# Optimization experiments

Measured on AMD Instinct MI355X. Metric: run time of the kernel, lower is better.

The kernel has to match this reference:

```python
import jax, jax.numpy as jnp
import numpy as np

M_COMP = 8      # number of output components m (n = m * tmax)
TMAX = 512
BS = 32
N = M_COMP * TMAX  # 4096


def setup_inputs() -> dict:
    key = jax.random.key(0)
    k1, k2, k3, k4 = jax.random.split(key, 4)
    # K must be symmetric positive definite for the Cholesky factorization.
    A = jax.random.normal(k1, (N, N), dtype=jnp.float32)
    K = A @ A.T / N + 1e-2 * jnp.eye(N, dtype=jnp.float32)
    # Sigma: diagonal measurement-noise covariance (positive diagonal).
    Sigma = jnp.diag(jax.random.uniform(k2, (N,), dtype=jnp.float32, minval=0.1, maxval=0.5))
    mu = jax.random.normal(k3, (N,), dtype=jnp.float32)
    Y = jax.random.normal(k4, (BS * N,), dtype=jnp.float32)
    return {"Y": Y, "mu": mu, "K": K, "Sigma": Sigma, "bs": BS, "tmax": TMAX}


def reference(Y, mu, K, Sigma, bs, tmax):
    n = mu.shape[0]  # m * tmax
    KS = K + Sigma
    # Chol_inv: inv = L^{-T} L^{-1} = (K + Sigma)^{-1}
    L = jnp.linalg.cholesky(KS)
    Linv = jnp.linalg.inv(L)
    inv = Linv.T @ Linv  # [n, n]
    # Block-diagonal quadratic form == sum of per-trajectory quadratic forms.
    diff = mu[None, :] - Y.reshape(bs, n)  # [bs, n]
    quad = jnp.einsum('bi,ij,bj->', diff, inv, diff)
    # log det(K + Sigma); slogdet is the stable equivalent (det > 0 for SPD).
    _, logdet = jnp.linalg.slogdet(KS)
    lml = (-quad / (2.0 * bs)
           - 0.5 * logdet
           - 0.5 * tmax * jnp.log(jnp.asarray(2.0 * np.pi, dtype=KS.dtype)))
    return -lml
```

## Files before the change

### kernel.cpp

```cpp
#include <hip/hip_runtime.h>
#include <math.h>

#define Nn 4096
#define BSc 32
#define NB 128
#define NBB 32
#define NBLK 33
#define NK 32
#define TILE_ELEMS (NB * NB)
#define NTILES 561

typedef float f32x4 __attribute__((ext_vector_type(4)));
typedef short bf16x8 __attribute__((ext_vector_type(8)));

__device__ __forceinline__ size_t tile_off(int i, int j) {
  return ((size_t)(j * NBLK - (j * (j - 1)) / 2 + (i - j))) * TILE_ELEMS;
}

__device__ __forceinline__ unsigned short f2bf(float f) {
  union { float f; unsigned int u; } v; v.f = f;
  unsigned int r = v.u + 0x7fffu + ((v.u >> 16) & 1u);
  return (unsigned short)(r >> 16);
}
__device__ __forceinline__ float bf2f(unsigned short b) {
  union { unsigned int u; float f; } v; v.u = ((unsigned int)b) << 16;
  return v.f;
}

__global__ __launch_bounds__(256) void prep(const float* __restrict__ Y,
                                            const float* __restrict__ mu,
                                            const float* __restrict__ Kp,
                                            const float* __restrict__ Sg,
                                            float* __restrict__ W) {
  int bid = blockIdx.x;
  int j = 0;
  while (j + 1 < NBLK) {
    int nxt = (j + 1) * NBLK - ((j + 1) * j) / 2;
    if (bid < nxt) break;
    ++j;
  }
  int start = j * NBLK - (j * (j - 1)) / 2;
  int i = j + (bid - start);
  float* T = W + tile_off(i, j);
  int tid = threadIdx.x;
  for (int idx = tid; idx < TILE_ELEMS; idx += 256) {
    int li = idx >> 7, lj = idx & 127;
    int gr = i * NB + li, gc = j * NB + lj;
    float v = 0.0f;
    if (gr < Nn) {
      v = Kp[(size_t)gr * Nn + gc];
      if (gr == gc) v += Sg[(size_t)gr * Nn + gr];
    } else {
      int b = gr - Nn;
      if (b < BSc && gc < Nn) v = mu[gc] - Y[(size_t)b * Nn + gc];
    }
    T[idx] = v;
  }
}

__global__ __launch_bounds__(256) void potf2(float* __restrict__ W, int k) {
  __shared__ float T[NB][NB + 1];
  __shared__ float dinv_sh[NBB];
  float* G = W + tile_off(k, k);
  int tid = threadIdx.x;
  for (int idx = tid; idx < TILE_ELEMS / 4; idx += 256) {
    float4 v = ((const float4*)G)[idx];
    int r = idx >> 5, c = (idx & 31) * 4;
    T[r][c] = v.x; T[r][c + 1] = v.y; T[r][c + 2] = v.z; T[r][c + 3] = v.w;
  }
  __syncthreads();
  int lane = tid & 63, wid = tid >> 6;
  for (int kb = 0; kb < 4; ++kb) {
    int o = kb * NBB;
    if (wid == 0) {
      int i = lane & 31;
      float cc[NBB];
#pragma unroll
      for (int p = 0; p < NBB; ++p) cc[p] = T[o + i][o + p];
#pragma unroll
      for (int j = 0; j < NBB; ++j) {
        float s = cc[j];
#pragma unroll
        for (int p = 0; p < NBB; ++p) {
          if (p < j) s -= cc[p] * __shfl(cc[p], j, 64);
        }
        float sj = __shfl(s, j, 64);
        float d = sqrtf(sj);
        if (i == j) cc[j] = d;
        else if (i > j) cc[j] = s / d;
      }
      if (lane < 32) {
#pragma unroll
        for (int p = 0; p < NBB; ++p) {
          if (p <= i) T[o + i][o + p] = cc[p];
        }
      }
    }
    __syncthreads();
    if (tid < NBB) dinv_sh[tid] = 1.0f / T[o + tid][o + tid];
    __syncthreads();
    int R = NB - o - NBB;
    if (R > 0) {
      if (tid < R) {
        int r = o + NBB + tid;
        float x[NBB];
#pragma unroll
        for (int p = 0; p < NBB; ++p) x[p] = T[r][o + p];
#pragma unroll
        for (int j = 0; j < NBB; ++j) {
          float s = x[j];
#pragma unroll
          for (int p = 0; p < NBB; ++p) {
            if (p < j) s -= x[p] * T[o + j][o + p];
          }
          x[j] = s * dinv_sh[j];
        }
#pragma unroll
        for (int p = 0; p < NBB; ++p) T[r][o + p] = x[p];
      }
      __syncthreads();
      int TL = R >> 2;
      int ntile = TL * (TL + 1) / 2;
      for (int t = tid; t < ntile; t += 256) {
        int ti = (int)((sqrtf(8.0f * t + 1.0f) - 1.0f) * 0.5f);
        while ((ti + 1) * (ti + 2) / 2 <= t) ++ti;
        while (ti * (ti + 1) / 2 > t) --ti;
        int tj = t - ti * (ti + 1) / 2;
        int tr = o + NBB + ti * 4, tc = o + NBB + tj * 4;
        float acc[4][4];
#pragma unroll
        for (int m = 0; m < 4; ++m)
#pragma unroll
          for (int n = 0; n < 4; ++n) acc[m][n] = 0.0f;
        for (int p = 0; p < NBB; ++p) {
          float a0 = T[tr][o + p], a1 = T[tr + 1][o + p],
                a2 = T[tr + 2][o + p], a3 = T[tr + 3][o + p];
          float b0 = T[tc][o + p], b1 = T[tc + 1][o + p],
                b2 = T[tc + 2][o + p], b3 = T[tc + 3][o + p];
          acc[0][0] += a0 * b0; acc[0][1] += a0 * b1; acc[0][2] += a0 * b2; acc[0][3] += a0 * b3;
          acc[1][0] += a1 * b0; acc[1][1] += a1 * b1; acc[1][2] += a1 * b2; acc[1][3] += a1 * b3;
          acc[2][0] += a2 * b0; acc[2][1] += a2 * b1; acc[2][2] += a2 * b2; acc[2][3] += a2 * b3;
          acc[3][0] += a3 * b0; acc[3][1] += a3 * b1; acc[3][2] += a3 * b2; acc[3][3] += a3 * b3;
        }
#pragma unroll
        for (int m = 0; m < 4; ++m)
#pragma unroll
          for (int n = 0; n < 4; ++n) T[tr + m][tc + n] -= acc[m][n];
      }
    }
    __syncthreads();
  }
  for (int idx = tid; idx < TILE_ELEMS; idx += 256) {
    int r = idx >> 7, c = idx & 127;
    if (c <= r) G[idx] = T[r][c];
  }
}

__global__ __launch_bounds__(256) void trsm(float* __restrict__ W,
                                            unsigned short* __restrict__ PH,
                                            unsigned short* __restrict__ PL,
                                            int k) {
  __shared__ float Td[NB][NB + 1];
  __shared__ float X[NB][NB + 1];
  __shared__ float dinv_sh[NB];
  int tid = threadIdx.x;
  int i = k + 1 + blockIdx.x;
  int rows = (i == NBLK - 1) ? BSc : NB;
  const float* Gd = W + tile_off(k, k);
  const float* Gx = W + tile_off(i, k);
  for (int idx = tid; idx < TILE_ELEMS / 4; idx += 256) {
    float4 v = ((const float4*)Gd)[idx];
    float4 u = ((const float4*)Gx)[idx];
    int r = idx >> 5, c = (idx & 31) * 4;
    Td[r][c] = v.x; Td[r][c + 1] = v.y; Td[r][c + 2] = v.z; Td[r][c + 3] = v.w;
    if (r < rows) { X[r][c] = u.x; X[r][c + 1] = u.y; X[r][c + 2] = u.z; X[r][c + 3] = u.w; }
    else          { X[r][c] = 0.0f; X[r][c + 1] = 0.0f; X[r][c + 2] = 0.0f; X[r][c + 3] = 0.0f; }
  }
  __syncthreads();
  if (tid < NB) dinv_sh[tid] = 1.0f / Td[tid][tid];
  __syncthreads();
  int rtile = (tid >> 3) * 4;
  int ctile = (tid & 7) * 4;
  for (int jb = 0; jb < 4; ++jb) {
    int o = jb * NBB;
    if (jb > 0) {
      float acc[4][4];
#pragma unroll
      for (int m = 0; m < 4; ++m)
#pragma unroll
        for (int n = 0; n < 4; ++n) acc[m][n] = 0.0f;
      for (int p = 0; p < o; ++p) {
        float a0 = X[rtile][p], a1 = X[rtile + 1][p],
              a2 = X[rtile + 2][p], a3 = X[rtile + 3][p];
        float b0 = Td[o + ctile][p], b1 = Td[o + ctile + 1][p],
              b2 = Td[o + ctile + 2][p], b3 = Td[o + ctile + 3][p];
        acc[0][0] += a0 * b0; acc[0][1] += a0 * b1; acc[0][2] += a0 * b2; acc[0][3] += a0 * b3;
        acc[1][0] += a1 * b0; acc[1][1] += a1 * b1; acc[1][2] += a1 * b2; acc[1][3] += a1 * b3;
        acc[2][0] += a2 * b0; acc[2][1] += a2 * b1; acc[2][2] += a2 * b2; acc[2][3] += a2 * b3;
        acc[3][0] += a3 * b0; acc[3][1] += a3 * b1; acc[3][2] += a3 * b2; acc[3][3] += a3 * b3;
      }
#pragma unroll
      for (int m = 0; m < 4; ++m)
#pragma unroll
        for (int n = 0; n < 4; ++n) X[rtile + m][o + ctile + n] -= acc[m][n];
      __syncthreads();
    }
    if (tid < NB) {
      int r = tid;
      float x[NBB];
#pragma unroll
      for (int p = 0; p < NBB; ++p) x[p] = X[r][o + p];
#pragma unroll
      for (int j = 0; j < NBB; ++j) {
        float s = x[j];
#pragma unroll
        for (int p = 0; p < NBB; ++p) {
          if (p < j) s -= x[p] * Td[o + j][o + p];
        }
        x[j] = s * dinv_sh[o + j];
      }
#pragma unroll
      for (int p = 0; p < NBB; ++p) X[r][o + p] = x[p];
    }
    __syncthreads();
  }
  int r = tid >> 1, hf = tid & 1;
  unsigned short* ph = PH + (size_t)i * TILE_ELEMS + (size_t)r * NB + hf * 64;
  unsigned short* pl = PL + (size_t)i * TILE_ELEMS + (size_t)r * NB + hf * 64;
#pragma unroll
  for (int ch = 0; ch < 8; ++ch) {
    unsigned short hb[8], lb[8];
#pragma unroll
    for (int e = 0; e < 8; ++e) {
      float v = X[r][hf * 64 + ch * 8 + e];
      unsigned short h = f2bf(v);
      hb[e] = h;
      lb[e] = f2bf(v - bf2f(h));
    }
    *reinterpret_cast<uint4*>(&ph[ch * 8]) = *reinterpret_cast<const uint4*>(hb);
    *reinterpret_cast<uint4*>(&pl[ch * 8]) = *reinterpret_cast<const uint4*>(lb);
  }
}

__global__ __launch_bounds__(256) void syrk(const unsigned short* __restrict__ PH,
                                            const unsigned short* __restrict__ PL,
                                            float* __restrict__ W, int k) {
  int i = k + 1 + blockIdx.x, j = k + 1 + blockIdx.y;
  if (i < j) return;
  const unsigned short* Ahg = PH + (size_t)i * TILE_ELEMS;
  const unsigned short* Alg = PL + (size_t)i * TILE_ELEMS;
  const unsigned short* Bhg = PH + (size_t)j * TILE_ELEMS;
  const unsigned short* Blg = PL + (size_t)j * TILE_ELEMS;
  float* C = W + tile_off(i, j);
  __shared__ unsigned short Ah[NB][40], Al[NB][40], Bh[NB][40], Bl[NB][40];
  int tid = threadIdx.x, lane = tid & 63, wid = tid >> 6;
  int wr = wid >> 1, wc = wid & 1, lm = lane & 15, lk = lane >> 4;
  f32x4 acc[4][4];
#pragma unroll
  for (int m = 0; m < 4; ++m)
#pragma unroll
    for (int n = 0; n < 4; ++n) acc[m][n] = (f32x4)0.0f;
  int r = tid >> 1, hf = tid & 1;
  for (int kb = 0; kb < 4; ++kb) {
    int kbase = kb * 32;
    if (kb) __syncthreads();
#pragma unroll
    for (int c = 0; c < 2; ++c) {
      int lc = (hf * 2 + c) * 8;
      int kc = kbase + lc;
      *reinterpret_cast<uint4*>(&Ah[r][lc]) = *reinterpret_cast<const uint4*>(&Ahg[(size_t)r * NB + kc]);
      *reinterpret_cast<uint4*>(&Al[r][lc]) = *reinterpret_cast<const uint4*>(&Alg[(size_t)r * NB + kc]);
      *reinterpret_cast<uint4*>(&Bh[r][lc]) = *reinterpret_cast<const uint4*>(&Bhg[(size_t)r * NB + kc]);
      *reinterpret_cast<uint4*>(&Bl[r][lc]) = *reinterpret_cast<const uint4*>(&Blg[(size_t)r * NB + kc]);
    }
    __syncthreads();
    bf16x8 ah[4], al[4], bh[4], bl[4];
#pragma unroll
    for (int mt = 0; mt < 4; ++mt) {
      int row = wr * 64 + mt * 16 + lm;
      ah[mt] = *reinterpret_cast<const bf16x8*>(&Ah[row][lk * 8]);
      al[mt] = *reinterpret_cast<const bf16x8*>(&Al[row][lk * 8]);
    }
#pragma unroll
    for (int nt = 0; nt < 4; ++nt) {
      int col = wc * 64 + nt * 16 + lm;
      bh[nt] = *reinterpret_cast<const bf16x8*>(&Bh[col][lk * 8]);
      bl[nt] = *reinterpret_cast<const bf16x8*>(&Bl[col][lk * 8]);
    }
#pragma unroll
    for (int mt = 0; mt < 4; ++mt)
#pragma unroll
      for (int nt = 0; nt < 4; ++nt) {
        acc[mt][nt] = __builtin_amdgcn_mfma_f32_16x16x32_bf16(ah[mt], bh[nt], acc[mt][nt], 0, 0, 0);
        acc[mt][nt] = __builtin_amdgcn_mfma_f32_16x16x32_bf16(al[mt], bh[nt], acc[mt][nt], 0, 0, 0);
        acc[mt][nt] = __builtin_amdgcn_mfma_f32_16x16x32_bf16(ah[mt], bl[nt], acc[mt][nt], 0, 0, 0);
      }
  }
#pragma unroll
  for (int mt = 0; mt < 4; ++mt)
#pragma unroll
    for (int nt = 0; nt < 4; ++nt) {
#pragma unroll
      for (int q = 0; q < 4; ++q) {
        int rr = wr * 64 + mt * 16 + lk * 4 + q;
        int cc = wc * 64 + nt * 16 + lm;
        C[rr * NB + cc] -= acc[mt][nt][q];
      }
    }
}

__global__ __launch_bounds__(256) void finalize(const float* __restrict__ W,
                                                const int* __restrict__ bsp,
                                                const int* __restrict__ tmaxp,
                                                float* __restrict__ out) {
  __shared__ float rl[4], rq[4];
  int tid = threadIdx.x;
  float lsum = 0.0f;
  for (int d = tid; d < Nn; d += 256) {
    int db = d >> 7, dl = d & 127;
    lsum += logf(W[tile_off(db, db) + (size_t)dl * NB + dl]);
  }
  float qsum = 0.0f;
  if (tid < BSc) qsum = W[tile_off(NBLK - 1, NBLK - 1) + (size_t)tid * NB + tid];
  for (int o = 32; o > 0; o >>= 1) {
    lsum += __shfl_down(lsum, o, 64);
    qsum += __shfl_down(qsum, o, 64);
  }
  int lane = tid & 63, wid = tid >> 6;
  if (lane == 0) { rl[wid] = lsum; rq[wid] = qsum; }
  __syncthreads();
  if (tid == 0) {
    float Lt = rl[0] + rl[1] + rl[2] + rl[3];
    float Qt = rq[0] + rq[1] + rq[2] + rq[3];
    float bsf = (float)bsp[0];
    float tmaxf = (float)tmaxp[0];
    out[0] = -Qt / (2.0f * bsf) + Lt + 0.5f * tmaxf * logf(6.283185307179586f);
  }
}

extern "C" void kernel_launch(void* const* d_in, const int* in_sizes, int n_in,
                              void* d_out, int out_size, void* d_ws, size_t ws_size,
                              hipStream_t stream) {
  const float* Y   = (const float*)d_in[0];
  const float* mu  = (const float*)d_in[1];
  const float* Kp  = (const float*)d_in[2];
  const float* Sg  = (const float*)d_in[3];
  const int*   bsp = (const int*)d_in[4];
  const int*   tmp_= (const int*)d_in[5];
  float* W = (float*)d_ws;
  unsigned short* PH = (unsigned short*)(W + (size_t)NTILES * TILE_ELEMS);
  unsigned short* PL = PH + (size_t)NBLK * TILE_ELEMS;
  float* out = (float*)d_out;

  prep<<<NTILES, 256, 0, stream>>>(Y, mu, Kp, Sg, W);

  for (int k = 0; k < NK; ++k) {
    potf2<<<1, 256, 0, stream>>>(W, k);
    int T = NBLK - (k + 1);
    trsm<<<T, 256, 0, stream>>>(W, PH, PL, k);
    dim3 g(T, T);
    syrk<<<g, 256, 0, stream>>>(PH, PL, W, k);
  }
  finalize<<<1, 256, 0, stream>>>(W, bsp, tmp_, out);
}
```

Baseline: 4.060 ms.

## Fuse diagonal-block Cholesky into TRSM panel kernel, recomputing per block

Removes the separate single-block potf2 launch. Each trsm block now redundantly factors the diagonal tile in shared memory before doing its triangular solve, and block 0 writes the diagonal into a side array Ld that finalize uses for the log-determinant. This cuts one serialized launch and one global round trip per step, in exchange for every block repeating the same factorization. Several loops also get unroll 1 pragmas, likely to limit register pressure in the larger fused kernel.

```diff
diff --git a/kernel.cpp b/kernel.cpp
--- a/kernel.cpp
+++ b/kernel.cpp
@@ -58,108 +58,11 @@
   }
 }
 
-__global__ __launch_bounds__(256) void potf2(float* __restrict__ W, int k) {
-  __shared__ float T[NB][NB + 1];
-  __shared__ float dinv_sh[NBB];
-  float* G = W + tile_off(k, k);
-  int tid = threadIdx.x;
-  for (int idx = tid; idx < TILE_ELEMS / 4; idx += 256) {
-    float4 v = ((const float4*)G)[idx];
-    int r = idx >> 5, c = (idx & 31) * 4;
-    T[r][c] = v.x; T[r][c + 1] = v.y; T[r][c + 2] = v.z; T[r][c + 3] = v.w;
-  }
-  __syncthreads();
-  int lane = tid & 63, wid = tid >> 6;
-  for (int kb = 0; kb < 4; ++kb) {
-    int o = kb * NBB;
-    if (wid == 0) {
-      int i = lane & 31;
-      float cc[NBB];
-#pragma unroll
-      for (int p = 0; p < NBB; ++p) cc[p] = T[o + i][o + p];
-#pragma unroll
-      for (int j = 0; j < NBB; ++j) {
-        float s = cc[j];
-#pragma unroll
-        for (int p = 0; p < NBB; ++p) {
-          if (p < j) s -= cc[p] * __shfl(cc[p], j, 64);
-        }
-        float sj = __shfl(s, j, 64);
-        float d = sqrtf(sj);
-        if (i == j) cc[j] = d;
-        else if (i > j) cc[j] = s / d;
-      }
-      if (lane < 32) {
-#pragma unroll
-        for (int p = 0; p < NBB; ++p) {
-          if (p <= i) T[o + i][o + p] = cc[p];
-        }
-      }
-    }
-    __syncthreads();
-    if (tid < NBB) dinv_sh[tid] = 1.0f / T[o + tid][o + tid];
-    __syncthreads();
-    int R = NB - o - NBB;
-    if (R > 0) {
-      if (tid < R) {
-        int r = o + NBB + tid;
-        float x[NBB];
-#pragma unroll
-        for (int p = 0; p < NBB; ++p) x[p] = T[r][o + p];
-#pragma unroll
-        for (int j = 0; j < NBB; ++j) {
-          float s = x[j];
-#pragma unroll
-          for (int p = 0; p < NBB; ++p) {
-            if (p < j) s -= x[p] * T[o + j][o + p];
-          }
-          x[j] = s * dinv_sh[j];
-        }
-#pragma unroll
-        for (int p = 0; p < NBB; ++p) T[r][o + p] = x[p];
-      }
-      __syncthreads();
-      int TL = R >> 2;
-      int ntile = TL * (TL + 1) / 2;
-      for (int t = tid; t < ntile; t += 256) {
-        int ti = (int)((sqrtf(8.0f * t + 1.0f) - 1.0f) * 0.5f);
-        while ((ti + 1) * (ti + 2) / 2 <= t) ++ti;
-        while (ti * (ti + 1) / 2 > t) --ti;
-        int tj = t - ti * (ti + 1) / 2;
-        int tr = o + NBB + ti * 4, tc = o + NBB + tj * 4;
-        float acc[4][4];
-#pragma unroll
-        for (int m = 0; m < 4; ++m)
-#pragma unroll
-          for (int n = 0; n < 4; ++n) acc[m][n] = 0.0f;
-        for (int p = 0; p < NBB; ++p) {
-          float a0 = T[tr][o + p], a1 = T[tr + 1][o + p],
-                a2 = T[tr + 2][o + p], a3 = T[tr + 3][o + p];
-          float b0 = T[tc][o + p], b1 = T[tc + 1][o + p],
-                b2 = T[tc + 2][o + p], b3 = T[tc + 3][o + p];
-          acc[0][0] += a0 * b0; acc[0][1] += a0 * b1; acc[0][2] += a0 * b2; acc[0][3] += a0 * b3;
-          acc[1][0] += a1 * b0; acc[1][1] += a1 * b1; acc[1][2] += a1 * b2; acc[1][3] += a1 * b3;
-          acc[2][0] += a2 * b0; acc[2][1] += a2 * b1; acc[2][2] += a2 * b2; acc[2][3] += a2 * b3;
-          acc[3][0] += a3 * b0; acc[3][1] += a3 * b1; acc[3][2] += a3 * b2; acc[3][3] += a3 * b3;
-        }
-#pragma unroll
-        for (int m = 0; m < 4; ++m)
-#pragma unroll
-          for (int n = 0; n < 4; ++n) T[tr + m][tc + n] -= acc[m][n];
-      }
-    }
-    __syncthreads();
-  }
-  for (int idx = tid; idx < TILE_ELEMS; idx += 256) {
-    int r = idx >> 7, c = idx & 127;
-    if (c <= r) G[idx] = T[r][c];
-  }
-}
-
-__global__ __launch_bounds__(256) void trsm(float* __restrict__ W,
-                                            unsigned short* __restrict__ PH,
-                                            unsigned short* __restrict__ PL,
-                                            int k) {
+__global__ __launch_bounds__(256) void panel(float* __restrict__ W,
+                                             unsigned short* __restrict__ PH,
+                                             unsigned short* __restrict__ PL,
+                                             float* __restrict__ Ld,
+                                             int k) {
   __shared__ float Td[NB][NB + 1];
   __shared__ float X[NB][NB + 1];
   __shared__ float dinv_sh[NB];
@@ -177,10 +80,97 @@
     else          { X[r][c] = 0.0f; X[r][c + 1] = 0.0f; X[r][c + 2] = 0.0f; X[r][c + 3] = 0.0f; }
   }
   __syncthreads();
-  if (tid < NB) dinv_sh[tid] = 1.0f / Td[tid][tid];
-  __syncthreads();
+  int lane = tid & 63, wid = tid >> 6;
+
+#pragma unroll 1
+  for (int kb = 0; kb < 4; ++kb) {
+    int o = kb * NBB;
+    if (wid == 0) {
+      int ii = lane & 31;
+      float cc[NBB];
+#pragma unroll
+      for (int p = 0; p < NBB; ++p) cc[p] = Td[o + ii][o + p];
+#pragma unroll
+      for (int j = 0; j < NBB; ++j) {
+        float s = cc[j];
+#pragma unroll
+        for (int p = 0; p < NBB; ++p) {
+          if (p < j) s -= cc[p] * __shfl(cc[p], j, 64);
+        }
+        float sj = __shfl(s, j, 64);
+        float d = sqrtf(sj);
+        if (ii == j) cc[j] = d;
+        else if (ii > j) cc[j] = s / d;
+      }
+      if (lane < 32) {
+#pragma unroll
+        for (int p = 0; p < NBB; ++p) {
+          if (p <= ii) Td[o + ii][o + p] = cc[p];
+        }
+      }
+    }
+    __syncthreads();
+    if (tid < NBB) dinv_sh[o + tid] = 1.0f / Td[o + tid][o + tid];
+    __syncthreads();
+    int R = NB - o - NBB;
+    if (R > 0) {
+      if (tid < R) {
+        int r = o + NBB + tid;
+        float x[NBB];
+#pragma unroll
+        for (int p = 0; p < NBB; ++p) x[p] = Td[r][o + p];
+#pragma unroll
+        for (int j = 0; j < NBB; ++j) {
+          float s = x[j];
+#pragma unroll
+          for (int p = 0; p < NBB; ++p) {
+            if (p < j) s -= x[p] * Td[o + j][o + p];
+          }
+          x[j] = s * dinv_sh[o + j];
+        }
+#pragma unroll
+        for (int p = 0; p < NBB; ++p) Td[r][o + p] = x[p];
+      }
+      __syncthreads();
+      int TL = R >> 2;
+      int ntile = TL * (TL + 1) / 2;
+#pragma unroll 1
+      for (int t = tid; t < ntile; t += 256) {
+        int ti = (int)((sqrtf(8.0f * t + 1.0f) - 1.0f) * 0.5f);
+        while ((ti + 1) * (ti + 2) / 2 <= t) ++ti;
+        while (ti * (ti + 1) / 2 > t) --ti;
+        int tj = t - ti * (ti + 1) / 2;
+        int tr = o + NBB + ti * 4, tc = o + NBB + tj * 4;
+        float acc[4][4];
+#pragma unroll
+        for (int m = 0; m < 4; ++m)
+#pragma unroll
+          for (int n = 0; n < 4; ++n) acc[m][n] = 0.0f;
+#pragma unroll 1
+        for (int p = 0; p < NBB; ++p) {
+          float a0 = Td[tr][o + p], a1 = Td[tr + 1][o + p],
+                a2 = Td[tr + 2][o + p], a3 = Td[tr + 3][o + p];
+          float b0 = Td[tc][o + p], b1 = Td[tc + 1][o + p],
+                b2 = Td[tc + 2][o + p], b3 = Td[tc + 3][o + p];
+          acc[0][0] += a0 * b0; acc[0][1] += a0 * b1; acc[0][2] += a0 * b2; acc[0][3] += a0 * b3;
+          acc[1][0] += a1 * b0; acc[1][1] += a1 * b1; acc[1][2] += a1 * b2; acc[1][3] += a1 * b3;
+          acc[2][0] += a2 * b0; acc[2][1] += a2 * b1; acc[2][2] += a2 * b2; acc[2][3] += a2 * b3;
+          acc[3][0] += a3 * b0; acc[3][1] += a3 * b1; acc[3][2] += a3 * b2; acc[3][3] += a3 * b3;
+        }
+#pragma unroll
+        for (int m = 0; m < 4; ++m)
+#pragma unroll
+          for (int n = 0; n < 4; ++n) Td[tr + m][tc + n] -= acc[m][n];
+      }
+    }
+    __syncthreads();
+  }
+
+  if (blockIdx.x == 0 && tid < NB) Ld[k * NB + tid] = Td[tid][tid];
+
   int rtile = (tid >> 3) * 4;
   int ctile = (tid & 7) * 4;
+#pragma unroll 1
   for (int jb = 0; jb < 4; ++jb) {
     int o = jb * NBB;
     if (jb > 0) {
@@ -189,6 +179,7 @@
       for (int m = 0; m < 4; ++m)
 #pragma unroll
         for (int n = 0; n < 4; ++n) acc[m][n] = 0.0f;
+#pragma unroll 1
       for (int p = 0; p < o; ++p) {
         float a0 = X[rtile][p], a1 = X[rtile + 1][p],
               a2 = X[rtile + 2][p], a3 = X[rtile + 3][p];
@@ -224,10 +215,11 @@
     }
     __syncthreads();
   }
+
   int r = tid >> 1, hf = tid & 1;
   unsigned short* ph = PH + (size_t)i * TILE_ELEMS + (size_t)r * NB + hf * 64;
   unsigned short* pl = PL + (size_t)i * TILE_ELEMS + (size_t)r * NB + hf * 64;
-#pragma unroll
+#pragma unroll 1
   for (int ch = 0; ch < 8; ++ch) {
     unsigned short hb[8], lb[8];
 #pragma unroll
@@ -261,6 +253,7 @@
 #pragma unroll
     for (int n = 0; n < 4; ++n) acc[m][n] = (f32x4)0.0f;
   int r = tid >> 1, hf = tid & 1;
+#pragma unroll 1
   for (int kb = 0; kb < 4; ++kb) {
     int kbase = kb * 32;
     if (kb) __syncthreads();
@@ -310,16 +303,14 @@
 }
 
 __global__ __launch_bounds__(256) void finalize(const float* __restrict__ W,
+                                                const float* __restrict__ Ld,
                                                 const int* __restrict__ bsp,
                                                 const int* __restrict__ tmaxp,
                                                 float* __restrict__ out) {
   __shared__ float rl[4], rq[4];
   int tid = threadIdx.x;
   float lsum = 0.0f;
-  for (int d = tid; d < Nn; d += 256) {
-    int db = d >> 7, dl = d & 127;
-    lsum += logf(W[tile_off(db, db) + (size_t)dl * NB + dl]);
-  }
+  for (int d = tid; d < Nn; d += 256) lsum += logf(Ld[d]);
   float qsum = 0.0f;
   if (tid < BSc) qsum = W[tile_off(NBLK - 1, NBLK - 1) + (size_t)tid * NB + tid];
   for (int o = 32; o > 0; o >>= 1) {
@@ -350,16 +341,16 @@
   float* W = (float*)d_ws;
   unsigned short* PH = (unsigned short*)(W + (size_t)NTILES * TILE_ELEMS);
   unsigned short* PL = PH + (size_t)NBLK * TILE_ELEMS;
+  float* Ld = (float*)(PL + (size_t)NBLK * TILE_ELEMS);
   float* out = (float*)d_out;
 
   prep<<<NTILES, 256, 0, stream>>>(Y, mu, Kp, Sg, W);
 
   for (int k = 0; k < NK; ++k) {
-    potf2<<<1, 256, 0, stream>>>(W, k);
     int T = NBLK - (k + 1);
-    trsm<<<T, 256, 0, stream>>>(W, PH, PL, k);
+    panel<<<T, 256, 0, stream>>>(W, PH, PL, Ld, k);
     dim3 g(T, T);
     syrk<<<g, 256, 0, stream>>>(PH, PL, W, k);
   }
-  finalize<<<1, 256, 0, stream>>>(W, bsp, tmp_, out);
-}
+  finalize<<<1, 256, 0, stream>>>(W, Ld, bsp, tmp_, out);
+}
```

After: 4.629 ms. 14.0% more time.
